# Optimization experiments

Hardware: AMD Instinct MI355X
Metric: run time of the kernel (lower is better)

The kernel has to match this reference:

```python
import jax, jax.numpy as jnp
import numpy as np

EMBED_DIM = 1024
NUM_HEADS = 16
HEAD_DIM = EMBED_DIM // NUM_HEADS
WINDOW = 128


def setup_inputs() -> dict:
    key = jax.random.key(0)
    ks = jax.random.split(key, 11)
    B, S, E = 2, 2048, EMBED_DIM
    scale = 1.0 / np.sqrt(E)
    inp = {
        "q": jax.random.normal(ks[0], (B, S, E), jnp.float32),
        "k": jax.random.normal(ks[1], (B, S, E), jnp.float32),
        "v": jax.random.normal(ks[2], (B, S, E), jnp.float32),
        "Wq": jax.random.normal(ks[3], (E, E), jnp.float32) * scale,
        "bq": jnp.zeros((E,), jnp.float32),
        "Wk": jax.random.normal(ks[4], (E, E), jnp.float32) * scale,
        "bk": jnp.zeros((E,), jnp.float32),
        "Wv": jax.random.normal(ks[5], (E, E), jnp.float32) * scale,
        "bv": jnp.zeros((E,), jnp.float32),
        "Wo": jax.random.normal(ks[6], (E, E), jnp.float32) * scale,
        "bo": jnp.zeros((E,), jnp.float32),
    }
    return inp


def reference(q, k, v, Wq, bq, Wk, bk, Wv, bv, Wo, bo):
    B, S, E = q.shape
    H, D = NUM_HEADS, HEAD_DIM
    # projections (torch Linear: x @ W.T + b)
    Q = (q @ Wq.T + bq).reshape(B, S, H, D).transpose(0, 2, 1, 3)  # [B,H,S,D]
    K = (k @ Wk.T + bk).reshape(B, S, H, D).transpose(0, 2, 1, 3)
    V = (v @ Wv.T + bv).reshape(B, S, H, D).transpose(0, 2, 1, 3)
    scores = jnp.einsum("bhqd,bhkd->bhqk", Q, K) / jnp.sqrt(jnp.float32(D))
    idx = jnp.arange(S)
    band = jnp.abs(idx[:, None] - idx[None, :]) <= WINDOW  # [S,S] bool band mask
    scores = jnp.where(band[None, None], scores, -jnp.inf)
    probs = jax.nn.softmax(scores, axis=-1)
    out = jnp.einsum("bhqk,bhkd->bhqd", probs, V)  # [B,H,S,D]
    out = out.transpose(0, 2, 1, 3).reshape(B, S, E)
    return out @ Wo.T + bo
```

## Files before the change

### kernel.cpp

```cpp
#include <hip/hip_runtime.h>


#define S_LEN 2048
#define EMB   1024
#define NHEAD 16
#define HDIM  64
#define MROWS 4096

typedef __attribute__((ext_vector_type(4))) float f32x4;
typedef __attribute__((ext_vector_type(8))) short bf16x8;

__device__ __forceinline__ unsigned short f2bf(float x){
  union { float f; unsigned u; } un; un.f = x;
  unsigned u = un.u;
  unsigned r = (u + 0x7FFFu + ((u >> 16) & 1u)) >> 16;
  return (unsigned short)r;
}

__global__ __launch_bounds__(256) void cvt7_kernel(
    const float4* __restrict__ q,  const float4* __restrict__ k,
    const float4* __restrict__ v,
    const float4* __restrict__ Wq, const float4* __restrict__ Wk,
    const float4* __restrict__ Wv, const float4* __restrict__ Wo,
    unsigned long long* __restrict__ dq, unsigned long long* __restrict__ dk,
    unsigned long long* __restrict__ dv,
    unsigned long long* __restrict__ dWq, unsigned long long* __restrict__ dWk,
    unsigned long long* __restrict__ dWv, unsigned long long* __restrict__ dWo)
{
  int i = blockIdx.x * 256 + threadIdx.x;
  int y = blockIdx.y;
  const float4* s;
  unsigned long long* d;
  int n4;
  switch (y){
    case 0: s = q;  d = dq;  n4 = 1048576; break;
    case 1: s = k;  d = dk;  n4 = 1048576; break;
    case 2: s = v;  d = dv;  n4 = 1048576; break;
    case 3: s = Wq; d = dWq; n4 = 262144;  break;
    case 4: s = Wk; d = dWk; n4 = 262144;  break;
    case 5: s = Wv; d = dWv; n4 = 262144;  break;
    default:s = Wo; d = dWo; n4 = 262144;  break;
  }
  if (i >= n4) return;
  float4 x = s[i];
  d[i] = (unsigned long long)f2bf(x.x)
       | ((unsigned long long)f2bf(x.y) << 16)
       | ((unsigned long long)f2bf(x.z) << 32)
       | ((unsigned long long)f2bf(x.w) << 48);
}

__device__ __forceinline__ void async_copy16(const unsigned short* g, unsigned short* l){
  __builtin_amdgcn_global_load_lds(
      (const __attribute__((address_space(1))) unsigned int*)(const void*)g,
      (__attribute__((address_space(3))) unsigned int*)(void*)l,
      16, 0, 0);
}

__device__ __forceinline__ void gemm_core_128(
    const unsigned short* __restrict__ A,
    const unsigned short* __restrict__ Bw,
    unsigned short* lds,
    int tile_m, int tile_n, f32x4 acc[4][4])
{
  const int tid  = threadIdx.x;
  const int lane = tid & 63;
  const int wid  = tid >> 6;
  const int wm = wid >> 1, wn = wid & 1;
  const int c = lane & 15, g = lane >> 4;
  const int srow = lane >> 3, sch = lane & 7;

  unsigned short* As0 = lds;
  unsigned short* Bs0 = lds + 8192;
  unsigned short* As1 = lds + 16384;
  unsigned short* Bs1 = lds + 24576;

  auto stage = [&](unsigned short* As, unsigned short* Bs, int k0){
#pragma unroll
    for (int i = 0; i < 4; ++i){
      int row = (wid*4 + i)*8 + srow;
      int chg = sch ^ (row & 7);
      async_copy16(A  + (size_t)(tile_m + row)*EMB + k0 + chg*8, As + (wid*4 + i)*512);
      async_copy16(Bw + (size_t)(tile_n + row)*EMB + k0 + chg*8, Bs + (wid*4 + i)*512);
    }
  };

  auto compute = [&](const unsigned short* As, const unsigned short* Bs){
#pragma unroll
    for (int kk = 0; kk < 2; ++kk){
      bf16x8 af[4], bfv[4];
#pragma unroll
      for (int mi = 0; mi < 4; ++mi){
        int row = wm*64 + mi*16 + c;
        int ch  = (kk*4 + g) ^ (row & 7);
        af[mi] = *(const bf16x8*)&As[row*64 + ch*8];
      }
#pragma unroll
      for (int ni = 0; ni < 4; ++ni){
        int row = wn*64 + ni*16 + c;
        int ch  = (kk*4 + g) ^ (row & 7);
        bfv[ni] = *(const bf16x8*)&Bs[row*64 + ch*8];
      }
#pragma unroll
      for (int mi = 0; mi < 4; ++mi)
#pragma unroll
        for (int ni = 0; ni < 4; ++ni)
          acc[mi][ni] = __builtin_amdgcn_mfma_f32_16x16x32_bf16(af[mi], bfv[ni], acc[mi][ni], 0, 0, 0);
    }
  };

  stage(As0, Bs0, 0);
  for (int t = 0; t < 16; ++t){
    const unsigned short* Ac = (t & 1) ? As1 : As0;
    const unsigned short* Bc = (t & 1) ? Bs1 : Bs0;
    unsigned short*       An = (t & 1) ? As0 : As1;
    unsigned short*       Bn = (t & 1) ? Bs0 : Bs1;
    if (t < 15){
      stage(An, Bn, (t + 1) * 64);
      asm volatile("s_waitcnt vmcnt(8)" ::: "memory");
    } else {
      asm volatile("s_waitcnt vmcnt(0)" ::: "memory");
    }
    asm volatile("s_barrier" ::: "memory");
    compute(Ac, Bc);
    asm volatile("s_barrier" ::: "memory");
  }
}

__global__ __launch_bounds__(256) void qkv_gemm_kernel(
    const unsigned short* __restrict__ qb, const unsigned short* __restrict__ kb2,
    const unsigned short* __restrict__ vb,
    const unsigned short* __restrict__ Wqb, const unsigned short* __restrict__ Wkb,
    const unsigned short* __restrict__ Wvb,
    const float* __restrict__ bq, const float* __restrict__ bk,
    const float* __restrict__ bv,
    unsigned short* __restrict__ Qp, unsigned short* __restrict__ Kp,
    unsigned short* __restrict__ Vt)
{
  __shared__ __align__(16) unsigned short lds[4*8192];
  const int z = blockIdx.z;
  const unsigned short* A    = (z == 0) ? qb  : (z == 1) ? kb2 : vb;
  const unsigned short* W    = (z == 0) ? Wqb : (z == 1) ? Wkb : Wvb;
  const float*          bias = (z == 0) ? bq  : (z == 1) ? bk  : bv;
  const int tile_m = blockIdx.x * 128;
  const int tile_n = blockIdx.y * 128;
  f32x4 acc[4][4] = {};
  gemm_core_128(A, W, lds, tile_m, tile_n, acc);

  const int tid = threadIdx.x, lane = tid & 63, wid = tid >> 6;
  const int wm = wid >> 1, wn = wid & 1, c = lane & 15, g = lane >> 4;

  if (z < 2){
    unsigned short* O = (z == 0) ? Qp : Kp;
#pragma unroll
    for (int mi = 0; mi < 4; ++mi){
      int m0 = tile_m + wm*64 + mi*16 + g*4;
#pragma unroll
      for (int ni = 0; ni < 4; ++ni){
        int n = tile_n + wn*64 + ni*16 + c;
        int h = n >> 6, d = n & 63;
        float bvn = bias[n];
#pragma unroll
        for (int j = 0; j < 4; ++j){
          int m = m0 + j;
          int bb = m >> 11, ss = m & 2047;
          O[(((size_t)bb*NHEAD + h)*S_LEN + ss)*HDIM + d] = f2bf(acc[mi][ni][j] + bvn);
        }
      }
    }
  } else {
#pragma unroll
    for (int mi = 0; mi < 4; ++mi){
      int m0 = tile_m + wm*64 + mi*16 + g*4;
      int bb = m0 >> 11, ss = m0 & 2047;
      int ssp = (ss & ~31) | (((ss >> 2) & 3) << 3) | (((ss >> 4) & 1) << 2);
#pragma unroll
      for (int ni = 0; ni < 4; ++ni){
        int n = tile_n + wn*64 + ni*16 + c;
        int h = n >> 6, d = n & 63;
        float bvn = bias[n];
        unsigned long long pk =
              (unsigned long long)f2bf(acc[mi][ni][0] + bvn)
            | ((unsigned long long)f2bf(acc[mi][ni][1] + bvn) << 16)
            | ((unsigned long long)f2bf(acc[mi][ni][2] + bvn) << 32)
            | ((unsigned long long)f2bf(acc[mi][ni][3] + bvn) << 48);
        *(unsigned long long*)&Vt[(((size_t)bb*NHEAD + h)*HDIM + d)*S_LEN + ssp] = pk;
      }
    }
  }
}

__global__ __launch_bounds__(256) void attn_kernel(
    const unsigned short* __restrict__ Qp, const unsigned short* __restrict__ Kp,
    const unsigned short* __restrict__ Vt, unsigned short* __restrict__ X2)
{
  __shared__ __align__(16) unsigned short Kl[2][64*64];
  __shared__ __align__(16) unsigned short Vl[2][64*64];

  const int tid = threadIdx.x, lane = tid & 63, w = tid >> 6;
  const int c = lane & 15, g = lane >> 4;
  int bid0 = blockIdx.x;
  int bid = (bid0 & 7) * 128 + (bid0 >> 3);
  const int bh = bid >> 5, qt = bid & 31;
  const int qbase = qt * 64;
  const int qw = qbase + w * 16;
  const int qi = qw + c;

  const unsigned short* Kbh = Kp + (size_t)bh * S_LEN * HDIM;
  const unsigned short* Vbh = Vt + (size_t)bh * HDIM * S_LEN;

  const unsigned short* Qb = Qp + ((size_t)bh*S_LEN + qw + c)*HDIM;
  bf16x8 aq0 = *(const bf16x8*)(Qb + g*8);
  bf16x8 aq1 = *(const bf16x8*)(Qb + 32 + g*8);

  f32x4 accO[4] = {};
  float lsum = 0.f;
  const float SC = 0.18033688011112042f;

  int t0 = qbase - 128; if (t0 < 0) t0 = 0;
  int t1 = qbase + 192; if (t1 > S_LEN) t1 = S_LEN;

  const int srow = lane >> 3;
  const int sch  = (lane & 7) ^ srow;

  auto stage = [&](int buf, int kt){
#pragma unroll
    for (int i = 0; i < 2; ++i){
      int r0 = w*16 + i*8;
      async_copy16(Kbh + (size_t)(kt + r0 + srow)*HDIM + sch*8, &Kl[buf][r0*64]);
      async_copy16(Vbh + (size_t)(r0 + srow)*S_LEN + kt + sch*8, &Vl[buf][r0*64]);
    }
  };

  auto compute = [&](int buf, int kt){
    f32x4 s[4];
    __builtin_amdgcn_s_setprio(1);
#pragma unroll
    for (int f = 0; f < 4; ++f){
      const unsigned short* Kr = &Kl[buf][(f*16 + c)*64];
      bf16x8 k0 = *(const bf16x8*)(Kr + ((    g) ^ (c & 7))*8);
      bf16x8 k1 = *(const bf16x8*)(Kr + ((4 + g) ^ (c & 7))*8);
      f32x4 a = {0.f, 0.f, 0.f, 0.f};
      a = __builtin_amdgcn_mfma_f32_16x16x32_bf16(k0, aq0, a, 0, 0, 0);
      a = __builtin_amdgcn_mfma_f32_16x16x32_bf16(k1, aq1, a, 0, 0, 0);
      s[f] = a;
    }
    __builtin_amdgcn_s_setprio(0);

    float p[4][4];
    bool nomask = (kt >= qw - 113) && (kt <= qw + 65);
    if (nomask){
#pragma unroll
      for (int f = 0; f < 4; ++f)
#pragma unroll
        for (int j = 0; j < 4; ++j){
          p[f][j] = exp2f(s[f][j] * SC);
          lsum += p[f][j];
        }
    } else {
#pragma unroll
      for (int f = 0; f < 4; ++f)
#pragma unroll
        for (int j = 0; j < 4; ++j){
          int dlt = qi - (kt + f*16 + g*4 + j);
          float e = exp2f(s[f][j] * SC);
          e = (dlt <= 128 && dlt >= -128) ? e : 0.f;
          p[f][j] = e;
          lsum += e;
        }
    }

    union { unsigned u[4]; bf16x8 v; } A0, A1;
    A0.u[0] = (unsigned)f2bf(p[0][0]) | ((unsigned)f2bf(p[0][1]) << 16);
    A0.u[1] = (unsigned)f2bf(p[0][2]) | ((unsigned)f2bf(p[0][3]) << 16);
    A0.u[2] = (unsigned)f2bf(p[1][0]) | ((unsigned)f2bf(p[1][1]) << 16);
    A0.u[3] = (unsigned)f2bf(p[1][2]) | ((unsigned)f2bf(p[1][3]) << 16);
    A1.u[0] = (unsigned)f2bf(p[2][0]) | ((unsigned)f2bf(p[2][1]) << 16);
    A1.u[1] = (unsigned)f2bf(p[2][2]) | ((unsigned)f2bf(p[2][3]) << 16);
    A1.u[2] = (unsigned)f2bf(p[3][0]) | ((unsigned)f2bf(p[3][1]) << 16);
    A1.u[3] = (unsigned)f2bf(p[3][2]) | ((unsigned)f2bf(p[3][3]) << 16);

    __builtin_amdgcn_s_setprio(1);
#pragma unroll
    for (int dblk = 0; dblk < 4; ++dblk){
      const unsigned short* Vr = &Vl[buf][(dblk*16 + c)*64];
      bf16x8 v0 = *(const bf16x8*)(Vr + ((    g) ^ (c & 7))*8);
      bf16x8 v1 = *(const bf16x8*)(Vr + ((4 + g) ^ (c & 7))*8);
      accO[dblk] = __builtin_amdgcn_mfma_f32_16x16x32_bf16(A0.v, v0, accO[dblk], 0, 0, 0);
      accO[dblk] = __builtin_amdgcn_mfma_f32_16x16x32_bf16(A1.v, v1, accO[dblk], 0, 0, 0);
    }
    __builtin_amdgcn_s_setprio(0);
  };

  stage(0, t0);
  int cur = 0;
  for (int kt = t0; kt < t1; kt += 64){
    if (kt + 64 < t1){
      stage(cur ^ 1, kt + 64);
      asm volatile("s_waitcnt vmcnt(4)" ::: "memory");
    } else {
      asm volatile("s_waitcnt vmcnt(0)" ::: "memory");
    }
    asm volatile("s_barrier" ::: "memory");
    bool active = (kt + 63 >= qw - 128) && (kt <= qw + 143);
    if (active) compute(cur, kt);
    asm volatile("s_barrier" ::: "memory");
    cur ^= 1;
  }

  lsum += __shfl_xor(lsum, 16);
  lsum += __shfl_xor(lsum, 32);
  float rl[4];
#pragma unroll
  for (int j = 0; j < 4; ++j)
    rl[j] = 1.f / __shfl(lsum, g*4 + j);

  const int b_ = bh >> 4, h_ = bh & 15;
#pragma unroll
  for (int dblk = 0; dblk < 4; ++dblk)
#pragma unroll
    for (int j = 0; j < 4; ++j){
      int s_ = qw + g*4 + j, d_ = dblk*16 + c;
      X2[((size_t)(b_*S_LEN + s_))*EMB + h_*64 + d_] = f2bf(accO[dblk][j] * rl[j]);
    }
}

__global__ __launch_bounds__(256) void out_gemm_kernel(
    const unsigned short* __restrict__ X2, const unsigned short* __restrict__ Wob,
    const float* __restrict__ bo, float* __restrict__ out)
{
  __shared__ __align__(16) unsigned short lds[4*8192];
  const int tile_m = blockIdx.x * 128;
  const int tile_n = blockIdx.y * 128;
  f32x4 acc[4][4] = {};
  gemm_core_128(X2, Wob, lds, tile_m, tile_n, acc);

  const int tid = threadIdx.x, lane = tid & 63, wid = tid >> 6;
  const int wm = wid >> 1, wn = wid & 1, c = lane & 15, g = lane >> 4;
#pragma unroll
  for (int mi = 0; mi < 4; ++mi){
    int m0 = tile_m + wm*64 + mi*16 + g*4;
#pragma unroll
    for (int ni = 0; ni < 4; ++ni){
      int n = tile_n + wn*64 + ni*16 + c;
      float bvn = bo[n];
#pragma unroll
      for (int j = 0; j < 4; ++j)
        out[(size_t)(m0 + j)*EMB + n] = acc[mi][ni][j] + bvn;
    }
  }
}

extern "C" void kernel_launch(void* const* d_in, const int* in_sizes, int n_in,
                              void* d_out, int out_size, void* d_ws, size_t ws_size,
                              hipStream_t stream)
{
  const float* q  = (const float*)d_in[0];
  const float* k  = (const float*)d_in[1];
  const float* v  = (const float*)d_in[2];
  const float* Wq = (const float*)d_in[3];
  const float* bq = (const float*)d_in[4];
  const float* Wk = (const float*)d_in[5];
  const float* bk = (const float*)d_in[6];
  const float* Wv = (const float*)d_in[7];
  const float* bv = (const float*)d_in[8];
  const float* Wo = (const float*)d_in[9];
  const float* bo = (const float*)d_in[10];
  float* out = (float*)d_out;

  unsigned short* ws = (unsigned short*)d_ws;
  unsigned short* qb  = ws;
  unsigned short* kb  = ws + 4194304;
  unsigned short* vb  = ws + 8388608;
  unsigned short* Wqb = ws + 12582912;
  unsigned short* Wkb = ws + 13631488;
  unsigned short* Wvb = ws + 14680064;
  unsigned short* Wob = ws + 15728640;
  unsigned short* Qp  = ws + 16777216;
  unsigned short* Kp  = ws + 20971520;
  unsigned short* Vt  = ws + 25165824;
  unsigned short* X2  = qb;

  cvt7_kernel<<<dim3(4096, 7), 256, 0, stream>>>(
      (const float4*)q, (const float4*)k, (const float4*)v,
      (const float4*)Wq, (const float4*)Wk, (const float4*)Wv, (const float4*)Wo,
      (unsigned long long*)qb, (unsigned long long*)kb, (unsigned long long*)vb,
      (unsigned long long*)Wqb, (unsigned long long*)Wkb,
      (unsigned long long*)Wvb, (unsigned long long*)Wob);

  qkv_gemm_kernel<<<dim3(32, 8, 3), 256, 0, stream>>>(
      qb, kb, vb, Wqb, Wkb, Wvb, bq, bk, bv, Qp, Kp, Vt);

  attn_kernel<<<1024, 256, 0, stream>>>(Qp, Kp, Vt, X2);

  out_gemm_kernel<<<dim3(32, 8), 256, 0, stream>>>(X2, Wob, bo, out);
}
```

Measured before the change: 88.72 us.

## Fuse fp32-to-bf16 activation conversion into QKV GEMM A-tile loads

The separate conversion pass no longer handles the q/k/v activations. The QKV GEMM now loads fp32 A tiles into registers, converts them to bf16 and writes them into swizzled LDS, while B tiles keep the async global-to-LDS path. This removes a full write and re-read of 24 MB of bf16 activations plus their conversion launch work. In exchange, each GEMM tile reads fp32 data (twice the bytes, re-read by 8 N-tiles), register pressure rises, and the pipeline now waits on vmcnt(0) every iteration.

```diff
diff --git a/kernel.cpp b/kernel.cpp
--- a/kernel.cpp
+++ b/kernel.cpp
@@ -17,36 +17,22 @@
   return (unsigned short)r;
 }
 
-__global__ __launch_bounds__(256) void cvt7_kernel(
-    const float4* __restrict__ q,  const float4* __restrict__ k,
-    const float4* __restrict__ v,
-    const float4* __restrict__ Wq, const float4* __restrict__ Wk,
-    const float4* __restrict__ Wv, const float4* __restrict__ Wo,
-    unsigned long long* __restrict__ dq, unsigned long long* __restrict__ dk,
-    unsigned long long* __restrict__ dv,
-    unsigned long long* __restrict__ dWq, unsigned long long* __restrict__ dWk,
-    unsigned long long* __restrict__ dWv, unsigned long long* __restrict__ dWo)
+__global__ __launch_bounds__(256) void cvt4_kernel(
+    const float4* __restrict__ s0, const float4* __restrict__ s1,
+    const float4* __restrict__ s2, const float4* __restrict__ s3,
+    unsigned long long* __restrict__ d0, unsigned long long* __restrict__ d1,
+    unsigned long long* __restrict__ d2, unsigned long long* __restrict__ d3)
 {
   int i = blockIdx.x * 256 + threadIdx.x;
-  int y = blockIdx.y;
-  const float4* s;
-  unsigned long long* d;
-  int n4;
-  switch (y){
-    case 0: s = q;  d = dq;  n4 = 1048576; break;
-    case 1: s = k;  d = dk;  n4 = 1048576; break;
-    case 2: s = v;  d = dv;  n4 = 1048576; break;
-    case 3: s = Wq; d = dWq; n4 = 262144;  break;
-    case 4: s = Wk; d = dWk; n4 = 262144;  break;
-    case 5: s = Wv; d = dWv; n4 = 262144;  break;
-    default:s = Wo; d = dWo; n4 = 262144;  break;
-  }
-  if (i >= n4) return;
-  float4 x = s[i];
-  d[i] = (unsigned long long)f2bf(x.x)
-       | ((unsigned long long)f2bf(x.y) << 16)
-       | ((unsigned long long)f2bf(x.z) << 32)
-       | ((unsigned long long)f2bf(x.w) << 48);
+  const float4* s = (blockIdx.y == 0) ? s0 : (blockIdx.y == 1) ? s1 :
+                    (blockIdx.y == 2) ? s2 : s3;
+  unsigned long long* d = (blockIdx.y == 0) ? d0 : (blockIdx.y == 1) ? d1 :
+                          (blockIdx.y == 2) ? d2 : d3;
+  float4 v = s[i];
+  d[i] = (unsigned long long)f2bf(v.x)
+       | ((unsigned long long)f2bf(v.y) << 16)
+       | ((unsigned long long)f2bf(v.z) << 32)
+       | ((unsigned long long)f2bf(v.w) << 48);
 }
 
 __device__ __forceinline__ void async_copy16(const unsigned short* g, unsigned short* l){
@@ -127,8 +113,8 @@
 }
 
 __global__ __launch_bounds__(256) void qkv_gemm_kernel(
-    const unsigned short* __restrict__ qb, const unsigned short* __restrict__ kb2,
-    const unsigned short* __restrict__ vb,
+    const float* __restrict__ qf, const float* __restrict__ kf,
+    const float* __restrict__ vf,
     const unsigned short* __restrict__ Wqb, const unsigned short* __restrict__ Wkb,
     const unsigned short* __restrict__ Wvb,
     const float* __restrict__ bq, const float* __restrict__ bk,
@@ -138,16 +124,102 @@
 {
   __shared__ __align__(16) unsigned short lds[4*8192];
   const int z = blockIdx.z;
-  const unsigned short* A    = (z == 0) ? qb  : (z == 1) ? kb2 : vb;
+  const float*          Af   = (z == 0) ? qf  : (z == 1) ? kf  : vf;
   const unsigned short* W    = (z == 0) ? Wqb : (z == 1) ? Wkb : Wvb;
   const float*          bias = (z == 0) ? bq  : (z == 1) ? bk  : bv;
   const int tile_m = blockIdx.x * 128;
   const int tile_n = blockIdx.y * 128;
+
+  const int tid  = threadIdx.x;
+  const int lane = tid & 63;
+  const int wid  = tid >> 6;
+  const int wm = wid >> 1, wn = wid & 1;
+  const int c = lane & 15, g = lane >> 4;
+  const int srow = lane >> 3, sch = lane & 7;
+
+  unsigned short* As0 = lds;
+  unsigned short* Bs0 = lds + 8192;
+  unsigned short* As1 = lds + 16384;
+  unsigned short* Bs1 = lds + 24576;
+
   f32x4 acc[4][4] = {};
-  gemm_core_128(A, W, lds, tile_m, tile_n, acc);
-
-  const int tid = threadIdx.x, lane = tid & 63, wid = tid >> 6;
-  const int wm = wid >> 1, wn = wid & 1, c = lane & 15, g = lane >> 4;
+  float4 areg[8];
+
+  auto loadA = [&](int k0){
+#pragma unroll
+    for (int i = 0; i < 4; ++i){
+      int C = (wid*4 + i)*64 + lane;
+      int r = C >> 3, cs = (C & 7) ^ (r & 7);
+      const float* src = Af + (size_t)(tile_m + r)*EMB + k0 + cs*8;
+      areg[i*2+0] = *(const float4*)(src);
+      areg[i*2+1] = *(const float4*)(src + 4);
+    }
+  };
+  auto writeA = [&](unsigned short* As){
+#pragma unroll
+    for (int i = 0; i < 4; ++i){
+      int C = (wid*4 + i)*64 + lane;
+      union { unsigned short s[8]; bf16x8 v; } u;
+      const float* f = (const float*)&areg[i*2];
+#pragma unroll
+      for (int j = 0; j < 8; ++j) u.s[j] = f2bf(f[j]);
+      *(bf16x8*)&As[C*8] = u.v;
+    }
+  };
+  auto stageB = [&](unsigned short* Bs, int k0){
+#pragma unroll
+    for (int i = 0; i < 4; ++i){
+      int row = (wid*4 + i)*8 + srow;
+      int chg = sch ^ (row & 7);
+      async_copy16(W + (size_t)(tile_n + row)*EMB + k0 + chg*8, Bs + (wid*4 + i)*512);
+    }
+  };
+  auto compute = [&](const unsigned short* As, const unsigned short* Bs){
+#pragma unroll
+    for (int kk = 0; kk < 2; ++kk){
+      bf16x8 af[4], bfv[4];
+#pragma unroll
+      for (int mi = 0; mi < 4; ++mi){
+        int row = wm*64 + mi*16 + c;
+        int ch  = (kk*4 + g) ^ (row & 7);
+        af[mi] = *(const bf16x8*)&As[row*64 + ch*8];
+      }
+#pragma unroll
+      for (int ni = 0; ni < 4; ++ni){
+        int row = wn*64 + ni*16 + c;
+        int ch  = (kk*4 + g) ^ (row & 7);
+        bfv[ni] = *(const bf16x8*)&Bs[row*64 + ch*8];
+      }
+#pragma unroll
+      for (int mi = 0; mi < 4; ++mi)
+#pragma unroll
+        for (int ni = 0; ni < 4; ++ni)
+          acc[mi][ni] = __builtin_amdgcn_mfma_f32_16x16x32_bf16(af[mi], bfv[ni], acc[mi][ni], 0, 0, 0);
+    }
+  };
+
+  loadA(0);
+  stageB(Bs0, 0);
+  writeA(As0);
+  asm volatile("s_waitcnt vmcnt(0) lgkmcnt(0)" ::: "memory");
+  asm volatile("s_barrier" ::: "memory");
+
+  for (int t = 0; t < 16; ++t){
+    const unsigned short* Ac = (t & 1) ? As1 : As0;
+    const unsigned short* Bc = (t & 1) ? Bs1 : Bs0;
+    unsigned short*       An = (t & 1) ? As0 : As1;
+    unsigned short*       Bn = (t & 1) ? Bs0 : Bs1;
+    if (t < 15){
+      loadA((t + 1) * 64);
+      stageB(Bn, (t + 1) * 64);
+    }
+    compute(Ac, Bc);
+    if (t < 15){
+      writeA(An);
+      asm volatile("s_waitcnt vmcnt(0) lgkmcnt(0)" ::: "memory");
+    }
+    asm volatile("s_barrier" ::: "memory");
+  }
 
   if (z < 2){
     unsigned short* O = (z == 0) ? Qp : Kp;
@@ -368,9 +440,7 @@
   float* out = (float*)d_out;
 
   unsigned short* ws = (unsigned short*)d_ws;
-  unsigned short* qb  = ws;
-  unsigned short* kb  = ws + 4194304;
-  unsigned short* vb  = ws + 8388608;
+  unsigned short* X2  = ws;
   unsigned short* Wqb = ws + 12582912;
   unsigned short* Wkb = ws + 13631488;
   unsigned short* Wvb = ws + 14680064;
@@ -378,17 +448,14 @@
   unsigned short* Qp  = ws + 16777216;
   unsigned short* Kp  = ws + 20971520;
   unsigned short* Vt  = ws + 25165824;
-  unsigned short* X2  = qb;
-
-  cvt7_kernel<<<dim3(4096, 7), 256, 0, stream>>>(
-      (const float4*)q, (const float4*)k, (const float4*)v,
+
+  cvt4_kernel<<<dim3(1024, 4), 256, 0, stream>>>(
       (const float4*)Wq, (const float4*)Wk, (const float4*)Wv, (const float4*)Wo,
-      (unsigned long long*)qb, (unsigned long long*)kb, (unsigned long long*)vb,
       (unsigned long long*)Wqb, (unsigned long long*)Wkb,
       (unsigned long long*)Wvb, (unsigned long long*)Wob);
 
   qkv_gemm_kernel<<<dim3(32, 8, 3), 256, 0, stream>>>(
-      qb, kb, vb, Wqb, Wkb, Wvb, bq, bk, bv, Qp, Kp, Vt);
+      q, k, v, Wqb, Wkb, Wvb, bq, bk, bv, Qp, Kp, Vt);
 
   attn_kernel<<<1024, 256, 0, stream>>>(Qp, Kp, Vt, X2);
 
```

After: 105.6 us. 19.0% more time.
